# Kernel tuning notes

Hardware: AMD Instinct MI355X
Metric: run time of the kernel (lower is better)

The kernel has to match this reference:

```python
import jax, jax.numpy as jnp
import numpy as np

K = 1024   # in_dim = out_dim = per-head dim (module uses full k per head)
H = 4      # heads
B, T = 2, 2048


def setup_inputs() -> dict:
    key = jax.random.key(0)
    ks = jax.random.split(key, 7)
    s = 0.02
    return {
        "x": jax.random.normal(ks[0], (B, T, K), jnp.float32),
        "Wq": jax.random.normal(ks[1], (K, K * H), jnp.float32) * s,
        "Wk": jax.random.normal(ks[2], (K, K * H), jnp.float32) * s,
        "Wv": jax.random.normal(ks[3], (K, K * H), jnp.float32) * s,
        "Wu": jax.random.normal(ks[4], (K * H, K), jnp.float32) * s,
        "bu": jnp.zeros((K,), jnp.float32),
        "W1": jax.random.normal(ks[5], (K, K), jnp.float32) * s,
        "b1": jnp.zeros((K,), jnp.float32),
        "W2": jax.random.normal(ks[6], (K, K), jnp.float32) * s,
        "b2": jnp.zeros((K,), jnp.float32),
    }


def reference(x, Wq, Wk, Wv, Wu, bu, W1, b1, W2, b2):
    b, t, k = x.shape
    h = H
    scale = k ** (-0.25)
    # projections: each head gets FULL dim k (quirk of the original module)
    q = (x @ Wq).reshape(b, t, h, k) * scale   # [b,t,h,k]
    kk = (x @ Wk).reshape(b, t, h, k) * scale
    v = (x @ Wv).reshape(b, t, h, k)
    # attention scores [b,h,q,k_pos]
    dot = jnp.einsum("bqhd,bkhd->bhqk", q, kk)
    causal = jnp.tril(jnp.ones((t, t), bool))  # strictly-upper masked to -inf
    dot = jnp.where(causal, dot, -jnp.inf)
    attn = jax.nn.softmax(dot, axis=-1)
    out = jnp.einsum("bhqk,bkhd->bqhd", attn, v).reshape(b, t, h * k)
    attn_out = out @ Wu + bu                   # unifyheads
    x = x + attn_out                            # residual
    ff = jax.nn.relu(x @ W1 + b1) @ W2 + b2     # in_dim == out_dim
    return x + ff                               # residual around FFN
```

## Files before the change

### kernel.cpp

```cpp
#include <hip/hip_runtime.h>
#include <math.h>


#define TM 128
#define TN 128

typedef __attribute__((ext_vector_type(8))) short short8;
typedef __attribute__((ext_vector_type(4))) float f32x4;

__device__ __forceinline__ unsigned short f2bf(float f) {
  union { float f; unsigned int u; } v; v.f = f;
  unsigned int r = (v.u + 0x7fffu + ((v.u >> 16) & 1u)) >> 16;
  return (unsigned short)r;
}
__device__ __forceinline__ float bf2f(unsigned short b) {
  union { unsigned int u; float f; } v; v.u = ((unsigned int)b) << 16;
  return v.f;
}

#define GL2LDS(g, l)                                                          \
  __builtin_amdgcn_global_load_lds(                                           \
      (__attribute__((address_space(1))) void*)(g),                           \
      (__attribute__((address_space(3))) void*)(l), 16, 0, 0)

__device__ __forceinline__ void gemm_core(
    const unsigned short* __restrict__ A, const unsigned short* __restrict__ BT,
    int m0, int n0, int kmax, int lda, int ldb, int ldc, long long coff,
    float scale, const float* __restrict__ bias,
    const float* __restrict__ resid, int do_relu, float* __restrict__ Cf,
    unsigned short* __restrict__ Cb, unsigned short* As, unsigned short* Bs) {
  const int tid = threadIdx.x;
  const int lane = tid & 63;
  const int wv = tid >> 6;
  const int wm = wv & 1;
  const int wn = wv >> 1;

  const int srow = tid >> 2;
  const int scol = (((tid & 3) ^ ((srow >> 1) & 3)) * 8);
  const unsigned short* ap0 = A + (long long)(m0 + srow) * lda + scol;
  const unsigned short* ap1 = ap0 + (long long)64 * lda;
  const unsigned short* bp0 = BT + (long long)(n0 + srow) * ldb + scol;
  const unsigned short* bp1 = bp0 + (long long)64 * ldb;
  unsigned short* lA = As + wv * 512;
  unsigned short* lB = Bs + wv * 512;

  f32x4 acc[4][4];
#pragma unroll
  for (int i = 0; i < 4; ++i)
#pragma unroll
    for (int j2 = 0; j2 < 4; ++j2) acc[i][j2] = {0.f, 0.f, 0.f, 0.f};

  const int frow = lane & 15;
  const int fqs = (((lane >> 4) ^ ((frow >> 1) & 3)) * 8);

  int rs = 0, rc = 0;

  auto stage = [&]() {
    unsigned short* a = lA + rs * 4096;
    unsigned short* b = lB + rs * 4096;
    GL2LDS(ap0, a); GL2LDS(ap1, a + 2048);
    GL2LDS(bp0, b); GL2LDS(bp1, b + 2048);
    ap0 += 32; ap1 += 32; bp0 += 32; bp1 += 32;
    rs ^= 1;
  };
  auto compute = [&]() {
    const unsigned short* Ac = As + rc * 4096;
    const unsigned short* Bc = Bs + rc * 4096;
    short8 afr[4], bfr[4];
#pragma unroll
    for (int mi = 0; mi < 4; ++mi)
      afr[mi] = *(const short8*)(Ac + (wm * 64 + mi * 16 + frow) * 32 + fqs);
#pragma unroll
    for (int ni = 0; ni < 4; ++ni)
      bfr[ni] = *(const short8*)(Bc + (wn * 64 + ni * 16 + frow) * 32 + fqs);
    __builtin_amdgcn_s_setprio(1);
#pragma unroll
    for (int mi = 0; mi < 4; ++mi)
#pragma unroll
      for (int ni = 0; ni < 4; ++ni)
        acc[mi][ni] = __builtin_amdgcn_mfma_f32_16x16x32_bf16(
            afr[mi], bfr[ni], acc[mi][ni], 0, 0, 0);
    __builtin_amdgcn_s_setprio(0);
    rc ^= 1;
  };

  const int nsteps = kmax >> 5;
  stage();
  for (int i = 0; i + 1 < nsteps; ++i) {
    stage();
    asm volatile("s_waitcnt vmcnt(4)" ::: "memory");
    __builtin_amdgcn_s_barrier();
    __builtin_amdgcn_sched_barrier(0);
    compute();
    __builtin_amdgcn_sched_barrier(0);
    __builtin_amdgcn_s_barrier();
  }
  asm volatile("s_waitcnt vmcnt(0)" ::: "memory");
  __builtin_amdgcn_s_barrier();
  __builtin_amdgcn_sched_barrier(0);
  compute();

  const int ccol = lane & 15;
  const int crow = (lane >> 4) * 4;
#pragma unroll
  for (int mi = 0; mi < 4; ++mi) {
#pragma unroll
    for (int ni = 0; ni < 4; ++ni) {
      const int gc = n0 + wn * 64 + ni * 16 + ccol;
#pragma unroll
      for (int r = 0; r < 4; ++r) {
        const int gr = m0 + wm * 64 + mi * 16 + crow + r;
        float v = acc[mi][ni][r] * scale;
        if (bias) v += bias[gc];
        if (resid) v += resid[(long long)gr * ldc + gc];
        if (do_relu) v = fmaxf(v, 0.f);
        const long long ci = coff + (long long)gr * ldc + gc;
        if (Cf) Cf[ci] = v;
        if (Cb) Cb[ci] = f2bf(v);
      }
    }
  }
}

__device__ __forceinline__ void core64(
    f32x4 acc[4][2], const unsigned short* __restrict__ A, int lda,
    const unsigned short* __restrict__ BT, int ldb, int kmax,
    unsigned short* As, unsigned short* Bs) {
  const int tid = threadIdx.x;
  const int lane = tid & 63;
  const int wv = tid >> 6;
  const int wm = wv & 1;
  const int wn = wv >> 1;
  const int srow = tid >> 2;
  const int scol = (((tid & 3) ^ ((srow >> 1) & 3)) * 8);
  const unsigned short* ap0 = A + (long long)srow * lda + scol;
  const unsigned short* ap1 = ap0 + (long long)64 * lda;
  const unsigned short* bp0 = BT + (long long)srow * ldb + scol;
  unsigned short* lA = As + wv * 512;
  unsigned short* lB = Bs + wv * 512;
  const int frow = lane & 15;
  const int fqs = (((lane >> 4) ^ ((frow >> 1) & 3)) * 8);

  int rs = 0, rc = 0;

  auto stage = [&]() {
    unsigned short* a = lA + rs * 4096;
    GL2LDS(ap0, a); GL2LDS(ap1, a + 2048);
    GL2LDS(bp0, lB + rs * 2048);
    ap0 += 32; ap1 += 32; bp0 += 32;
    rs ^= 1;
  };
  auto compute = [&]() {
    const unsigned short* Ac = As + rc * 4096;
    const unsigned short* Bc = Bs + rc * 2048;
    short8 afr[4], bfr[2];
#pragma unroll
    for (int mi = 0; mi < 4; ++mi)
      afr[mi] = *(const short8*)(Ac + (wm * 64 + mi * 16 + frow) * 32 + fqs);
#pragma unroll
    for (int ni = 0; ni < 2; ++ni)
      bfr[ni] = *(const short8*)(Bc + (wn * 32 + ni * 16 + frow) * 32 + fqs);
    __builtin_amdgcn_s_setprio(1);
#pragma unroll
    for (int mi = 0; mi < 4; ++mi)
#pragma unroll
      for (int ni = 0; ni < 2; ++ni)
        acc[mi][ni] = __builtin_amdgcn_mfma_f32_16x16x32_bf16(
            afr[mi], bfr[ni], acc[mi][ni], 0, 0, 0);
    __builtin_amdgcn_s_setprio(0);
    rc ^= 1;
  };

  const int nsteps = kmax >> 5;
  stage();
  for (int i = 0; i + 1 < nsteps; ++i) {
    stage();
    asm volatile("s_waitcnt vmcnt(3)" ::: "memory");
    __builtin_amdgcn_s_barrier();
    __builtin_amdgcn_sched_barrier(0);
    compute();
    __builtin_amdgcn_sched_barrier(0);
    __builtin_amdgcn_s_barrier();
  }
  asm volatile("s_waitcnt vmcnt(0)" ::: "memory");
  __builtin_amdgcn_s_barrier();
  __builtin_amdgcn_sched_barrier(0);
  compute();
}

__global__ __launch_bounds__(256) void gemm_ffn(
    const unsigned short* __restrict__ A, const unsigned short* __restrict__ BT,
    const float* __restrict__ bias, const float* __restrict__ resid,
    int do_relu, float* __restrict__ Cf, unsigned short* __restrict__ Cb) {
  __shared__ unsigned short As[8192];
  __shared__ unsigned short Bs[4096];
  const int bid = blockIdx.x;
  const int xcd = bid & 7;
  const int j = bid >> 3;
  const int m0 = (xcd * 4 + (j & 3)) * 128;
  const int n0 = (j >> 2) * 64;
  f32x4 acc[4][2];
#pragma unroll
  for (int i = 0; i < 4; ++i)
#pragma unroll
    for (int j2 = 0; j2 < 2; ++j2) acc[i][j2] = {0.f, 0.f, 0.f, 0.f};
  core64(acc, A + (long long)m0 * 1024, 1024, BT + (long long)n0 * 1024, 1024,
         1024, As, Bs);
  const int lane = threadIdx.x & 63;
  const int wv = threadIdx.x >> 6;
  const int wm = wv & 1, wn = wv >> 1;
  const int ccol = lane & 15, crow = (lane >> 4) * 4;
#pragma unroll
  for (int mi = 0; mi < 4; ++mi) {
#pragma unroll
    for (int ni = 0; ni < 2; ++ni) {
      const int gc = n0 + wn * 32 + ni * 16 + ccol;
#pragma unroll
      for (int r = 0; r < 4; ++r) {
        const int gr = m0 + wm * 64 + mi * 16 + crow + r;
        float v = acc[mi][ni][r] + bias[gc];
        if (resid) v += resid[(long long)gr * 1024 + gc];
        if (do_relu) v = fmaxf(v, 0.f);
        const long long ci = (long long)gr * 1024 + gc;
        if (Cf) Cf[ci] = v;
        if (Cb) Cb[ci] = f2bf(v);
      }
    }
  }
}

__global__ __launch_bounds__(256) void gemm_bt(
    const unsigned short* __restrict__ A, const unsigned short* __restrict__ BT,
    int Kd, int lda, int ldb, int ldc, int bh_shift,
    long long aob, long long aoh, long long bob, long long boh,
    long long cob, long long coh, float scale,
    const float* __restrict__ bias, const float* __restrict__ resid,
    int do_relu, float* __restrict__ Cf, unsigned short* __restrict__ Cb,
    int causal_mode, int grid_mode) {
  __shared__ unsigned short As[8192];
  __shared__ unsigned short Bs[8192];
  int n0, m0, z;
  if (grid_mode == 2) {
    z = blockIdx.x; n0 = blockIdx.y * TN; m0 = blockIdx.z * TM;
  } else if (grid_mode == 4) {
    z = blockIdx.x; m0 = blockIdx.y * TM; n0 = blockIdx.z * TN;
  } else {
    n0 = blockIdx.x * TN; m0 = blockIdx.y * TM; z = blockIdx.z;
  }

  const int zb = z >> bh_shift;
  const int zh = z & ((1 << bh_shift) - 1);
  const long long aoff = (long long)zb * aob + (long long)zh * aoh;
  const long long boff = (long long)zb * bob + (long long)zh * boh;
  const long long coff = (long long)zb * cob + (long long)zh * coh;

  int kmax = Kd;
  if (causal_mode == 2) { int t = m0 + TM; if (t < kmax) kmax = t; }

  gemm_core(A + aoff, BT + boff, m0, n0, kmax, lda, ldb, ldc, coff, scale,
            bias, resid, do_relu, Cf, Cb, As, Bs);
}

__global__ __launch_bounds__(256) void gemm_t(
    const unsigned short* __restrict__ xb,
    const unsigned short* __restrict__ Wcomb,
    unsigned short* __restrict__ tb) {
  __shared__ unsigned short As[8192];
  __shared__ unsigned short Bs[8192];
  const int bid = blockIdx.x;
  const int xcd = bid & 7;
  const int j = bid >> 3;
  const int m0 = (xcd * 4 + (j & 3)) * TM;
  const int n0 = (j >> 2) * TN;
  gemm_core(xb, Wcomb, m0, n0, 1024, 1024, 1024, 4096, 0, 1.0f,
            nullptr, nullptr, 0, nullptr, tb, As, Bs);
}

__global__ __launch_bounds__(256) void gemm_sv(
    const unsigned short* __restrict__ xb,
    const unsigned short* __restrict__ Wcomb,
    const unsigned short* __restrict__ tb,
    unsigned short* __restrict__ S, unsigned short* __restrict__ vT) {
  __shared__ unsigned short As[8192];
  __shared__ unsigned short Bs[8192];
  const long long TT = (long long)2048 * 2048;
  const int bid = blockIdx.x;
  if (bid < 1088) {
    const int z = bid & 7, zb = z >> 2, zh = z & 3;
    const int idx = bid >> 3;
    int m = (int)((sqrtf(8.0f * idx + 1.0f) - 1.0f) * 0.5f);
    while ((m + 1) * (m + 2) / 2 <= idx) ++m;
    while (m * (m + 1) / 2 > idx) --m;
    const int m0 = m * TM;
    const int n0 = (idx - m * (m + 1) / 2) * TN;
    gemm_core(tb + (long long)zb * 2048 * 4096 + zh * 1024,
              xb + (long long)zb * 2048 * 1024,
              m0, n0, 1024, 4096, 1024, 2048,
              (long long)zb * 4 * TT + (long long)zh * TT,
              1.0f, nullptr, nullptr, 0, nullptr, S, As, Bs);
  } else {
    const int r = bid - 1088;
    const int xcd = r & 7;
    const int j = r >> 3;
    const int bb = j >> 6;
    const int rr = j & 63;
    const int m0 = (xcd * 4 + (rr & 3)) * TM;
    const int n0 = (rr >> 2) * TN;
    gemm_core(Wcomb + (size_t)4096 * 1024, xb + (long long)bb * 2048 * 1024,
              m0, n0, 1024, 1024, 1024, 2048, (long long)bb * 4096 * 2048,
              1.0f, nullptr, nullptr, 0, nullptr, vT, As, Bs);
  }
}

__global__ __launch_bounds__(256) void reduce_epi(
    const unsigned short* __restrict__ Pb, int S, long long MN,
    const float* __restrict__ bias, const float* __restrict__ resid,
    int do_relu, float* __restrict__ Cf, unsigned short* __restrict__ Cb) {
  const long long i4 = ((long long)blockIdx.x * 256 + threadIdx.x) * 4;
  if (i4 >= MN) return;
  float4 s = {0.f, 0.f, 0.f, 0.f};
  for (int t = 0; t < S; ++t) {
    const ushort4 p = *(const ushort4*)(Pb + (long long)t * MN + i4);
    s.x += bf2f(p.x); s.y += bf2f(p.y); s.z += bf2f(p.z); s.w += bf2f(p.w);
  }
  if (bias) {
    const int c0 = (int)(i4 & 1023);
    s.x += bias[c0]; s.y += bias[c0 + 1]; s.z += bias[c0 + 2]; s.w += bias[c0 + 3];
  }
  if (resid) {
    const float4 rr = *(const float4*)(resid + i4);
    s.x += rr.x; s.y += rr.y; s.z += rr.z; s.w += rr.w;
  }
  if (do_relu) {
    s.x = fmaxf(s.x, 0.f); s.y = fmaxf(s.y, 0.f);
    s.z = fmaxf(s.z, 0.f); s.w = fmaxf(s.w, 0.f);
  }
  if (Cf) *(float4*)(Cf + i4) = s;
  if (Cb) {
    ushort4 o;
    o.x = f2bf(s.x); o.y = f2bf(s.y); o.z = f2bf(s.z); o.w = f2bf(s.w);
    *(ushort4*)(Cb + i4) = o;
  }
}

__global__ __launch_bounds__(256) void softmax_causal(unsigned short* S, int T) {
  const int q = blockIdx.x;
  unsigned short* row = S + ((long long)blockIdx.y * T + q) * T;
  const int tid = threadIdx.x;
  const int lane = tid & 63;
  const int wv = tid >> 6;
  const int n = q + 1;
  const int nz = (n + 127) & ~127;
  const int base = tid * 8;
  short8 raw = {};
  if (base < nz) raw = *(const short8*)(row + base);
  float vals[8];
  float m = -__builtin_inff();
#pragma unroll
  for (int i = 0; i < 8; ++i) {
    vals[i] = (base + i < n) ? bf2f((unsigned short)raw[i]) : -__builtin_inff();
    m = fmaxf(m, vals[i]);
  }
#pragma unroll
  for (int o = 32; o; o >>= 1) m = fmaxf(m, __shfl_xor(m, o, 64));
  __shared__ float red[4];
  if (lane == 0) red[wv] = m;
  __syncthreads();
  m = fmaxf(fmaxf(red[0], red[1]), fmaxf(red[2], red[3]));
  __syncthreads();
  float s = 0.f, e[8];
#pragma unroll
  for (int i = 0; i < 8; ++i) {
    e[i] = (base + i < n) ? __expf(vals[i] - m) : 0.f;
    s += e[i];
  }
#pragma unroll
  for (int o = 32; o; o >>= 1) s += __shfl_xor(s, o, 64);
  if (lane == 0) red[wv] = s;
  __syncthreads();
  s = red[0] + red[1] + red[2] + red[3];
  const float inv = 1.f / s;
  if (base < nz) {
    short8 o8;
#pragma unroll
    for (int i = 0; i < 8; ++i) o8[i] = (short)f2bf(e[i] * inv);
    *(short8*)(row + base) = o8;
  }
}

__global__ __launch_bounds__(256) void prep_all(
    const float* __restrict__ x, const float* __restrict__ Wq,
    const float* __restrict__ Wk, const float* __restrict__ Wv,
    const float* __restrict__ Wu, const float* __restrict__ W1,
    const float* __restrict__ W2, unsigned short* __restrict__ xb,
    unsigned short* __restrict__ Wqc, unsigned short* __restrict__ Wkc,
    unsigned short* __restrict__ Wvc, unsigned short* __restrict__ WuTb,
    unsigned short* __restrict__ W1T, unsigned short* __restrict__ W2T,
    float s2) {
  const int z = blockIdx.y;
  if (z <= 3) {
    const float* src = (z == 0) ? x : (z == 1) ? Wq : (z == 2) ? Wk : Wv;
    unsigned short* dst = (z == 0) ? xb : (z == 1) ? Wqc : (z == 2) ? Wkc : Wvc;
    const float sc = (z == 2) ? s2 : 1.0f;
    const long long i4 = ((long long)blockIdx.x * 256 + threadIdx.x) * 4;
    const float4 v = *(const float4*)(src + i4);
    ushort4 u;
    u.x = f2bf(v.x * sc); u.y = f2bf(v.y * sc);
    u.z = f2bf(v.z * sc); u.w = f2bf(v.w * sc);
    *(ushort4*)(dst + i4) = u;
    return;
  }
  const int R = (z == 4) ? 4096 : 1024;
  const int by = blockIdx.x >> 5;
  if (by * 32 >= R) return;
  const float* W = (z == 4) ? Wu : (z == 5) ? W1 : W2;
  unsigned short* WT = (z == 4) ? WuTb : (z == 5) ? W1T : W2T;
  __shared__ float tile[32][33];
  const int c0 = (blockIdx.x & 31) * 32;
  const int r0 = by * 32;
  const int tx = threadIdx.x & 31;
  const int ty = threadIdx.x >> 5;
#pragma unroll
  for (int j = 0; j < 32; j += 8)
    tile[ty + j][tx] = W[(long long)(r0 + ty + j) * 1024 + c0 + tx];
  __syncthreads();
#pragma unroll
  for (int j = 0; j < 32; j += 8)
    WT[(long long)(c0 + ty + j) * R + r0 + tx] = f2bf(tile[tx][ty + j]);
}

extern "C" void kernel_launch(void* const* d_in, const int* in_sizes, int n_in,
                              void* d_out, int out_size, void* d_ws,
                              size_t ws_size, hipStream_t stream) {
  (void)in_sizes; (void)n_in; (void)out_size; (void)ws_size;
  const float* x  = (const float*)d_in[0];
  const float* Wq = (const float*)d_in[1];
  const float* Wk = (const float*)d_in[2];
  const float* Wv = (const float*)d_in[3];
  const float* Wu = (const float*)d_in[4];
  const float* bu = (const float*)d_in[5];
  const float* W1 = (const float*)d_in[6];
  const float* b1 = (const float*)d_in[7];
  const float* W2 = (const float*)d_in[8];
  const float* b2 = (const float*)d_in[9];
  float* out = (float*)d_out;

  const int T = 2048, K = 1024;
  const size_t MB = 1024 * 1024;
  const long long MN = (long long)4096 * 1024;
  const long long TT = (long long)T * T;
  const long long Mi = 1024 * 1024;

  char* w = (char*)d_ws;
  unsigned short* xb    = (unsigned short*)(w + 0 * MB);
  unsigned short* Wqc   = (unsigned short*)(w + 8 * MB);
  unsigned short* Wvc   = (unsigned short*)(w + 16 * MB);
  unsigned short* Wkc   = (unsigned short*)(w + 24 * MB);
  unsigned short* WuTb  = (unsigned short*)(w + 32 * MB);
  unsigned short* Wcomb = (unsigned short*)(w + 40 * MB);
  unsigned short* tb    = (unsigned short*)(w + 56 * MB);
  unsigned short* vT    = (unsigned short*)(w + 88 * MB);
  unsigned short* S     = (unsigned short*)(w + 120 * MB);
  unsigned short* W1T   = (unsigned short*)(w + 184 * MB);
  unsigned short* W2T   = (unsigned short*)(w + 186 * MB);
  unsigned short* Pb    = (unsigned short*)(w + 40 * MB);
  float*          x1f   = (float*)(w + 8 * MB);
  unsigned short* x1b   = (unsigned short*)(w + 24 * MB);
  unsigned short* h1    = (unsigned short*)(w + 32 * MB);

  const float s2 = 0.03125f;

  prep_all<<<dim3(4096, 7), 256, 0, stream>>>(
      x, Wq, Wk, Wv, Wu, W1, W2, xb, Wqc, Wkc, Wvc, WuTb, W1T, W2T, s2);

  gemm_bt<<<dim3(8, 8, 8), 256, 0, stream>>>(
      Wkc, Wqc, K, 4096, 4096, 1024, 2,
      4 * Mi, 1024, 4 * Mi, 1024, 4 * Mi, Mi, 1.0f,
      nullptr, nullptr, 0, nullptr, Wcomb, 0, 2);

  gemm_t<<<dim3(1024), 256, 0, stream>>>(xb, Wcomb, tb);

  gemm_sv<<<dim3(2112), 256, 0, stream>>>(xb, Wcomb, tb, S, vT);

  softmax_causal<<<dim3(T, 8), 256, 0, stream>>>(S, T);

  gemm_bt<<<dim3(8, T / TM, K / TN), 256, 0, stream>>>(
      S, vT, T, T, 2048, K, 2,
      (long long)4 * TT, TT, (long long)4096 * 2048, (long long)1024 * 2048,
      (long long)2048 * 1024, MN, 1.0f,
      nullptr, nullptr, 0, nullptr, Pb, 2, 4);

  reduce_epi<<<dim3(4096), 256, 0, stream>>>(Pb, 4, MN, bu, x, 0, x1f, x1b);

  gemm_ffn<<<dim3(512), 256, 0, stream>>>(x1b, W1T, b1, nullptr, 1,
                                          nullptr, h1);

  gemm_ffn<<<dim3(512), 256, 0, stream>>>(h1, W2T, b2, x1f, 0, out, nullptr);
}
```

Before: 441.8 us.

## Replace 128x128 GEMM tiles with 256x256 eight-wave core for attention GEMMs

Replaces the 128x128, 4-wave GEMM core with a 256x256-tile, 8-wave core. It uses 64-wide K steps, double-buffered 128KB LDS, and a four-quadrant schedule that interleaves prefetch of the next K tile with MFMA work. The combine, t, S/vT and PV GEMMs get dedicated kernels with remapped grids, and the softmax zero-pad granularity moves to 256 to match the causal tile size. Larger tiles raise arithmetic intensity and cut global traffic. In exchange there are fewer blocks (occupancy risk), more causal over-computation, and higher register pressure.

```diff
diff --git a/kernel.cpp b/kernel.cpp
--- a/kernel.cpp
+++ b/kernel.cpp
@@ -1,9 +1,6 @@
 #include <hip/hip_runtime.h>
 #include <math.h>
 
-
-#define TM 128
-#define TN 128
 
 typedef __attribute__((ext_vector_type(8))) short short8;
 typedef __attribute__((ext_vector_type(4))) float f32x4;
@@ -23,103 +20,223 @@
       (__attribute__((address_space(1))) void*)(g),                           \
       (__attribute__((address_space(3))) void*)(l), 16, 0, 0)
 
-__device__ __forceinline__ void gemm_core(
+__device__ __forceinline__ void core256(
     const unsigned short* __restrict__ A, const unsigned short* __restrict__ BT,
     int m0, int n0, int kmax, int lda, int ldb, int ldc, long long coff,
-    float scale, const float* __restrict__ bias,
-    const float* __restrict__ resid, int do_relu, float* __restrict__ Cf,
-    unsigned short* __restrict__ Cb, unsigned short* As, unsigned short* Bs) {
+    unsigned short* __restrict__ Cb, unsigned short* lds) {
   const int tid = threadIdx.x;
   const int lane = tid & 63;
-  const int wv = tid >> 6;
-  const int wm = wv & 1;
-  const int wn = wv >> 1;
-
-  const int srow = tid >> 2;
-  const int scol = (((tid & 3) ^ ((srow >> 1) & 3)) * 8);
-  const unsigned short* ap0 = A + (long long)(m0 + srow) * lda + scol;
-  const unsigned short* ap1 = ap0 + (long long)64 * lda;
-  const unsigned short* bp0 = BT + (long long)(n0 + srow) * ldb + scol;
-  const unsigned short* bp1 = bp0 + (long long)64 * ldb;
-  unsigned short* lA = As + wv * 512;
-  unsigned short* lB = Bs + wv * 512;
-
-  f32x4 acc[4][4];
-#pragma unroll
-  for (int i = 0; i < 4; ++i)
-#pragma unroll
-    for (int j2 = 0; j2 < 4; ++j2) acc[i][j2] = {0.f, 0.f, 0.f, 0.f};
+  const int wid = tid >> 6;
+  const int wm = wid >> 2;
+  const int wn = wid & 3;
+
+  unsigned short* Als = lds;
+  unsigned short* Bls = lds + 32768;
+
+  const int srow = wid * 8 + (lane >> 3);
+  const int scol = ((lane & 7) ^ (lane >> 3)) * 8;
+  const unsigned short* ag = A + (long long)(m0 + srow) * lda + scol;
+  const unsigned short* bg = BT + (long long)(n0 + srow) * ldb + scol;
 
   const int frow = lane & 15;
-  const int fqs = (((lane >> 4) ^ ((frow >> 1) & 3)) * 8);
-
-  int rs = 0, rc = 0;
-
-  auto stage = [&]() {
-    unsigned short* a = lA + rs * 4096;
-    unsigned short* b = lB + rs * 4096;
-    GL2LDS(ap0, a); GL2LDS(ap1, a + 2048);
-    GL2LDS(bp0, b); GL2LDS(bp1, b + 2048);
-    ap0 += 32; ap1 += 32; bp0 += 32; bp1 += 32;
-    rs ^= 1;
+  const int lq = lane >> 4;
+  const int fsw = frow & 7;
+
+  f32x4 acc[8][4];
+#pragma unroll
+  for (int i = 0; i < 8; ++i)
+#pragma unroll
+    for (int j = 0; j < 4; ++j) acc[i][j] = {0.f, 0.f, 0.f, 0.f};
+
+  short8 afr[4][2];
+  short8 bfrE[2][2];
+  short8 bfrO[2][2];
+
+  const int NT = kmax >> 6;
+
+  auto stageA = [&](int t_, int h_) {
+    unsigned short* d = Als + (t_ & 1) * 16384 + h_ * 8192 + wid * 512;
+    const unsigned short* g = ag + ((long long)h_ * 128) * lda + t_ * 64;
+    GL2LDS(g, d);
+    GL2LDS(g + (long long)64 * lda, d + 4096);
   };
-  auto compute = [&]() {
-    const unsigned short* Ac = As + rc * 4096;
-    const unsigned short* Bc = Bs + rc * 4096;
-    short8 afr[4], bfr[4];
-#pragma unroll
-    for (int mi = 0; mi < 4; ++mi)
-      afr[mi] = *(const short8*)(Ac + (wm * 64 + mi * 16 + frow) * 32 + fqs);
-#pragma unroll
-    for (int ni = 0; ni < 4; ++ni)
-      bfr[ni] = *(const short8*)(Bc + (wn * 64 + ni * 16 + frow) * 32 + fqs);
-    __builtin_amdgcn_s_setprio(1);
-#pragma unroll
-    for (int mi = 0; mi < 4; ++mi)
-#pragma unroll
-      for (int ni = 0; ni < 4; ++ni)
-        acc[mi][ni] = __builtin_amdgcn_mfma_f32_16x16x32_bf16(
-            afr[mi], bfr[ni], acc[mi][ni], 0, 0, 0);
-    __builtin_amdgcn_s_setprio(0);
-    rc ^= 1;
+  auto stageB = [&](int t_, int h_) {
+    unsigned short* d = Bls + (t_ & 1) * 16384 + h_ * 8192 + wid * 512;
+    const unsigned short* g = bg + ((long long)h_ * 128) * ldb + t_ * 64;
+    GL2LDS(g, d);
+    GL2LDS(g + (long long)64 * ldb, d + 4096);
   };
 
-  const int nsteps = kmax >> 5;
-  stage();
-  for (int i = 0; i + 1 < nsteps; ++i) {
-    stage();
-    asm volatile("s_waitcnt vmcnt(4)" ::: "memory");
-    __builtin_amdgcn_s_barrier();
-    __builtin_amdgcn_sched_barrier(0);
-    compute();
-    __builtin_amdgcn_sched_barrier(0);
-    __builtin_amdgcn_s_barrier();
-  }
-  asm volatile("s_waitcnt vmcnt(0)" ::: "memory");
-  __builtin_amdgcn_s_barrier();
-  __builtin_amdgcn_sched_barrier(0);
-  compute();
+#define RDA(QM)                                                               \
+  _Pragma("unroll")                                                           \
+  for (int m_ = 0; m_ < 4; ++m_)                                              \
+    _Pragma("unroll")                                                         \
+    for (int kh_ = 0; kh_ < 2; ++kh_)                                         \
+      afr[m_][kh_] = *(const short8*)(Als + b * 16384 + wm * 8192 +           \
+          ((QM) * 64 + m_ * 16 + frow) * 64 + ((kh_ * 4 + lq) ^ fsw) * 8);
+
+#define RDB(QN, BFR)                                                          \
+  _Pragma("unroll")                                                           \
+  for (int n_ = 0; n_ < 2; ++n_)                                              \
+    _Pragma("unroll")                                                         \
+    for (int kh_ = 0; kh_ < 2; ++kh_)                                         \
+      BFR[n_][kh_] = *(const short8*)(Bls + b * 16384 + (wn >> 1) * 8192 +    \
+          ((wn & 1) * 64 + (QN) * 32 + n_ * 16 + frow) * 64 +                 \
+          ((kh_ * 4 + lq) ^ fsw) * 8);
+
+#define QUAD(QM, QN, BFR)                                                     \
+  do {                                                                        \
+    __builtin_amdgcn_s_setprio(1);                                            \
+    _Pragma("unroll")                                                         \
+    for (int m_ = 0; m_ < 4; ++m_)                                            \
+      _Pragma("unroll")                                                       \
+      for (int n_ = 0; n_ < 2; ++n_)                                          \
+        _Pragma("unroll")                                                     \
+        for (int kh_ = 0; kh_ < 2; ++kh_)                                     \
+          acc[(QM) * 4 + m_][(QN) * 2 + n_] =                                 \
+              __builtin_amdgcn_mfma_f32_16x16x32_bf16(                        \
+                  afr[m_][kh_], BFR[n_][kh_],                                 \
+                  acc[(QM) * 4 + m_][(QN) * 2 + n_], 0, 0, 0);                \
+    __builtin_amdgcn_s_setprio(0);                                            \
+  } while (0)
+
+  stageA(0, 0); stageA(0, 1); stageB(0, 0); stageB(0, 1);
+
+  for (int t = 0; t < NT; ++t) {
+    const int b = t & 1;
+    const bool pf = (t + 1 < NT);
+    if (pf) {
+      stageA(t + 1, 0);
+      asm volatile("s_waitcnt vmcnt(2)" ::: "memory");
+    } else {
+      asm volatile("s_waitcnt vmcnt(0)" ::: "memory");
+    }
+    __builtin_amdgcn_s_barrier();
+    RDA(0)
+    RDB(0, bfrE)
+    asm volatile("s_waitcnt lgkmcnt(0)" ::: "memory");
+    __builtin_amdgcn_sched_barrier(0);
+    QUAD(0, 0, bfrE);
+    __builtin_amdgcn_sched_barrier(0);
+    __builtin_amdgcn_s_barrier();
+    RDB(1, bfrO)
+    if (pf) stageB(t + 1, 0);
+    __builtin_amdgcn_s_barrier();
+    asm volatile("s_waitcnt lgkmcnt(0)" ::: "memory");
+    __builtin_amdgcn_sched_barrier(0);
+    QUAD(0, 1, bfrO);
+    __builtin_amdgcn_sched_barrier(0);
+    __builtin_amdgcn_s_barrier();
+    RDA(1)
+    if (pf) stageA(t + 1, 1);
+    __builtin_amdgcn_s_barrier();
+    asm volatile("s_waitcnt lgkmcnt(0)" ::: "memory");
+    __builtin_amdgcn_sched_barrier(0);
+    QUAD(1, 1, bfrO);
+    __builtin_amdgcn_sched_barrier(0);
+    __builtin_amdgcn_s_barrier();
+    if (pf) stageB(t + 1, 1);
+    __builtin_amdgcn_s_barrier();
+    QUAD(1, 0, bfrE);
+    __builtin_amdgcn_sched_barrier(0);
+    __builtin_amdgcn_s_barrier();
+  }
+#undef RDA
+#undef RDB
+#undef QUAD
 
   const int ccol = lane & 15;
-  const int crow = (lane >> 4) * 4;
-#pragma unroll
-  for (int mi = 0; mi < 4; ++mi) {
+  const int crow = lq * 4;
+#pragma unroll
+  for (int mi = 0; mi < 8; ++mi) {
 #pragma unroll
     for (int ni = 0; ni < 4; ++ni) {
       const int gc = n0 + wn * 64 + ni * 16 + ccol;
 #pragma unroll
       for (int r = 0; r < 4; ++r) {
-        const int gr = m0 + wm * 64 + mi * 16 + crow + r;
-        float v = acc[mi][ni][r] * scale;
-        if (bias) v += bias[gc];
-        if (resid) v += resid[(long long)gr * ldc + gc];
-        if (do_relu) v = fmaxf(v, 0.f);
-        const long long ci = coff + (long long)gr * ldc + gc;
-        if (Cf) Cf[ci] = v;
-        if (Cb) Cb[ci] = f2bf(v);
+        const int gr = m0 + wm * 128 + mi * 16 + crow + r;
+        Cb[coff + (long long)gr * ldc + gc] = f2bf(acc[mi][ni][r]);
       }
     }
   }
+}
+
+
+__global__ __launch_bounds__(512, 2) void g256_cmb(
+    const unsigned short* __restrict__ Wkc,
+    const unsigned short* __restrict__ Wqc,
+    unsigned short* __restrict__ Wcomb) {
+  __shared__ unsigned short lds[65536];
+  const long long Mi = 1024 * 1024;
+  const int bid = blockIdx.x;
+  const int z = bid & 7, zb = z >> 2, zh = z & 3;
+  const int j = bid >> 3;
+  const int m0 = (j & 3) * 256, n0 = (j >> 2) * 256;
+  core256(Wkc + (long long)zb * 4 * Mi + zh * 1024,
+          Wqc + (long long)zb * 4 * Mi + zh * 1024,
+          m0, n0, 1024, 4096, 4096, 1024,
+          (long long)zb * 4 * Mi + (long long)zh * Mi, Wcomb, lds);
+}
+
+__global__ __launch_bounds__(512, 2) void g256_t(
+    const unsigned short* __restrict__ xb,
+    const unsigned short* __restrict__ Wcomb,
+    unsigned short* __restrict__ tb) {
+  __shared__ unsigned short lds[65536];
+  const int bid = blockIdx.x;
+  const int xcd = bid & 7;
+  const int j = bid >> 3;
+  const int m0 = (xcd * 2 + (j & 1)) * 256;
+  const int n0 = (j >> 1) * 256;
+  core256(xb, Wcomb, m0, n0, 1024, 1024, 1024, 4096, 0, tb, lds);
+}
+
+__global__ __launch_bounds__(512, 2) void g256_sv(
+    const unsigned short* __restrict__ xb,
+    const unsigned short* __restrict__ Wcomb,
+    const unsigned short* __restrict__ tb,
+    unsigned short* __restrict__ S, unsigned short* __restrict__ vT) {
+  __shared__ unsigned short lds[65536];
+  const long long TT = (long long)2048 * 2048;
+  const int bid = blockIdx.x;
+  if (bid < 288) {
+    const int z = bid & 7, zb = z >> 2, zh = z & 3;
+    const int idx = bid >> 3;
+    int m = (int)((sqrtf(8.0f * idx + 1.0f) - 1.0f) * 0.5f);
+    while ((m + 1) * (m + 2) / 2 <= idx) ++m;
+    while (m * (m + 1) / 2 > idx) --m;
+    const int m0 = m * 256;
+    const int n0 = (idx - m * (m + 1) / 2) * 256;
+    core256(tb + (long long)zb * 2048 * 4096 + zh * 1024,
+            xb + (long long)zb * 2048 * 1024,
+            m0, n0, 1024, 4096, 1024, 2048,
+            (long long)(zb * 4 + zh) * TT, S, lds);
+  } else {
+    const int r = bid - 288;
+    const int xcd = r & 7;
+    const int j = r >> 3;
+    const int m0 = (xcd * 2 + (j & 1)) * 256;
+    const int rest = j >> 1;
+    const int bb = rest >> 3;
+    const int n0 = (rest & 7) * 256;
+    core256(Wcomb + (size_t)4096 * 1024, xb + (long long)bb * 2048 * 1024,
+            m0, n0, 1024, 1024, 1024, 2048, (long long)bb * 4096 * 2048,
+            vT, lds);
+  }
+}
+
+__global__ __launch_bounds__(512, 2) void g256_pv(
+    const unsigned short* __restrict__ S, const unsigned short* __restrict__ vT,
+    unsigned short* __restrict__ Pb) {
+  __shared__ unsigned short lds[65536];
+  const long long TT = (long long)2048 * 2048;
+  const long long MN = (long long)4096 * 1024;
+  const int z = blockIdx.x, zb = z >> 2, zh = z & 3;
+  const int m0 = blockIdx.y * 256, n0 = blockIdx.z * 256;
+  core256(S + (long long)(zb * 4 + zh) * TT,
+          vT + (long long)zb * 4096 * 2048 + (long long)zh * 1024 * 2048,
+          m0, n0, m0 + 256, 2048, 2048, 1024,
+          (long long)zh * MN + (long long)zb * 2048 * 1024, Pb, lds);
 }
 
 __device__ __forceinline__ void core64(
@@ -229,89 +346,6 @@
   }
 }
 
-__global__ __launch_bounds__(256) void gemm_bt(
-    const unsigned short* __restrict__ A, const unsigned short* __restrict__ BT,
-    int Kd, int lda, int ldb, int ldc, int bh_shift,
-    long long aob, long long aoh, long long bob, long long boh,
-    long long cob, long long coh, float scale,
-    const float* __restrict__ bias, const float* __restrict__ resid,
-    int do_relu, float* __restrict__ Cf, unsigned short* __restrict__ Cb,
-    int causal_mode, int grid_mode) {
-  __shared__ unsigned short As[8192];
-  __shared__ unsigned short Bs[8192];
-  int n0, m0, z;
-  if (grid_mode == 2) {
-    z = blockIdx.x; n0 = blockIdx.y * TN; m0 = blockIdx.z * TM;
-  } else if (grid_mode == 4) {
-    z = blockIdx.x; m0 = blockIdx.y * TM; n0 = blockIdx.z * TN;
-  } else {
-    n0 = blockIdx.x * TN; m0 = blockIdx.y * TM; z = blockIdx.z;
-  }
-
-  const int zb = z >> bh_shift;
-  const int zh = z & ((1 << bh_shift) - 1);
-  const long long aoff = (long long)zb * aob + (long long)zh * aoh;
-  const long long boff = (long long)zb * bob + (long long)zh * boh;
-  const long long coff = (long long)zb * cob + (long long)zh * coh;
-
-  int kmax = Kd;
-  if (causal_mode == 2) { int t = m0 + TM; if (t < kmax) kmax = t; }
-
-  gemm_core(A + aoff, BT + boff, m0, n0, kmax, lda, ldb, ldc, coff, scale,
-            bias, resid, do_relu, Cf, Cb, As, Bs);
-}
-
-__global__ __launch_bounds__(256) void gemm_t(
-    const unsigned short* __restrict__ xb,
-    const unsigned short* __restrict__ Wcomb,
-    unsigned short* __restrict__ tb) {
-  __shared__ unsigned short As[8192];
-  __shared__ unsigned short Bs[8192];
-  const int bid = blockIdx.x;
-  const int xcd = bid & 7;
-  const int j = bid >> 3;
-  const int m0 = (xcd * 4 + (j & 3)) * TM;
-  const int n0 = (j >> 2) * TN;
-  gemm_core(xb, Wcomb, m0, n0, 1024, 1024, 1024, 4096, 0, 1.0f,
-            nullptr, nullptr, 0, nullptr, tb, As, Bs);
-}
-
-__global__ __launch_bounds__(256) void gemm_sv(
-    const unsigned short* __restrict__ xb,
-    const unsigned short* __restrict__ Wcomb,
-    const unsigned short* __restrict__ tb,
-    unsigned short* __restrict__ S, unsigned short* __restrict__ vT) {
-  __shared__ unsigned short As[8192];
-  __shared__ unsigned short Bs[8192];
-  const long long TT = (long long)2048 * 2048;
-  const int bid = blockIdx.x;
-  if (bid < 1088) {
-    const int z = bid & 7, zb = z >> 2, zh = z & 3;
-    const int idx = bid >> 3;
-    int m = (int)((sqrtf(8.0f * idx + 1.0f) - 1.0f) * 0.5f);
-    while ((m + 1) * (m + 2) / 2 <= idx) ++m;
-    while (m * (m + 1) / 2 > idx) --m;
-    const int m0 = m * TM;
-    const int n0 = (idx - m * (m + 1) / 2) * TN;
-    gemm_core(tb + (long long)zb * 2048 * 4096 + zh * 1024,
-              xb + (long long)zb * 2048 * 1024,
-              m0, n0, 1024, 4096, 1024, 2048,
-              (long long)zb * 4 * TT + (long long)zh * TT,
-              1.0f, nullptr, nullptr, 0, nullptr, S, As, Bs);
-  } else {
-    const int r = bid - 1088;
-    const int xcd = r & 7;
-    const int j = r >> 3;
-    const int bb = j >> 6;
-    const int rr = j & 63;
-    const int m0 = (xcd * 4 + (rr & 3)) * TM;
-    const int n0 = (rr >> 2) * TN;
-    gemm_core(Wcomb + (size_t)4096 * 1024, xb + (long long)bb * 2048 * 1024,
-              m0, n0, 1024, 1024, 1024, 2048, (long long)bb * 4096 * 2048,
-              1.0f, nullptr, nullptr, 0, nullptr, vT, As, Bs);
-  }
-}
-
 __global__ __launch_bounds__(256) void reduce_epi(
     const unsigned short* __restrict__ Pb, int S, long long MN,
     const float* __restrict__ bias, const float* __restrict__ resid,
@@ -350,7 +384,7 @@
   const int lane = tid & 63;
   const int wv = tid >> 6;
   const int n = q + 1;
-  const int nz = (n + 127) & ~127;
+  const int nz = (n + 255) & ~255;
   const int base = tid * 8;
   short8 raw = {};
   if (base < nz) raw = *(const short8*)(row + base);
@@ -445,11 +479,9 @@
   const float* b2 = (const float*)d_in[9];
   float* out = (float*)d_out;
 
-  const int T = 2048, K = 1024;
+  const int T = 2048;
   const size_t MB = 1024 * 1024;
   const long long MN = (long long)4096 * 1024;
-  const long long TT = (long long)T * T;
-  const long long Mi = 1024 * 1024;
 
   char* w = (char*)d_ws;
   unsigned short* xb    = (unsigned short*)(w + 0 * MB);
@@ -467,28 +499,22 @@
   float*          x1f   = (float*)(w + 8 * MB);
   unsigned short* x1b   = (unsigned short*)(w + 24 * MB);
   unsigned short* h1    = (unsigned short*)(w + 32 * MB);
+  (void)WuTb; (void)Wvc;
 
   const float s2 = 0.03125f;
 
   prep_all<<<dim3(4096, 7), 256, 0, stream>>>(
       x, Wq, Wk, Wv, Wu, W1, W2, xb, Wqc, Wkc, Wvc, WuTb, W1T, W2T, s2);
 
-  gemm_bt<<<dim3(8, 8, 8), 256, 0, stream>>>(
-      Wkc, Wqc, K, 4096, 4096, 1024, 2,
-      4 * Mi, 1024, 4 * Mi, 1024, 4 * Mi, Mi, 1.0f,
-      nullptr, nullptr, 0, nullptr, Wcomb, 0, 2);
-
-  gemm_t<<<dim3(1024), 256, 0, stream>>>(xb, Wcomb, tb);
-
-  gemm_sv<<<dim3(2112), 256, 0, stream>>>(xb, Wcomb, tb, S, vT);
+  g256_cmb<<<dim3(128), 512, 0, stream>>>(Wkc, Wqc, Wcomb);
+
+  g256_t<<<dim3(256), 512, 0, stream>>>(xb, Wcomb, tb);
+
+  g256_sv<<<dim3(544), 512, 0, stream>>>(xb, Wcomb, tb, S, vT);
 
   softmax_causal<<<dim3(T, 8), 256, 0, stream>>>(S, T);
 
-  gemm_bt<<<dim3(8, T / TM, K / TN), 256, 0, stream>>>(
-      S, vT, T, T, 2048, K, 2,
-      (long long)4 * TT, TT, (long long)4096 * 2048, (long long)1024 * 2048,
-      (long long)2048 * 1024, MN, 1.0f,
-      nullptr, nullptr, 0, nullptr, Pb, 2, 4);
+  g256_pv<<<dim3(8, 8, 4), 512, 0, stream>>>(S, vT, Pb);
 
   reduce_epi<<<dim3(4096), 256, 0, stream>>>(Pb, 4, MN, bu, x, 0, x1f, x1b);
 
```

Result: faster. 420.0 us (-4.9%).
